# Kernel optimization log

Hardware: AMD Instinct MI355X
Metric: run time of the kernel (lower is better)

## Reference

```python
import jax, jax.numpy as jnp
import numpy as np

B, T, N, H = 256, 64, 128, 128  # batch, seq_len, num_tasks, hidden_dim


def setup_inputs() -> dict:
    key = jax.random.key(0)
    k = jax.random.split(key, 8)
    task_seq = jax.random.randint(k[0], (B, T), 0, N)
    status_seq = jax.random.randint(k[1], (B, T), 0, 3)
    raw = (jax.random.uniform(k[2], (N, N)) < 0.05).astype(jnp.float32)
    adj = raw + jnp.eye(N, dtype=jnp.float32)
    rs = adj.sum(axis=1, keepdims=True)
    adj = adj / jnp.where(rs == 0, 1.0, rs)
    s = np.float32(1.0 / np.sqrt(H))
    emb = jax.random.normal(k[3], (N * 3, H), jnp.float32) * s      # interaction_emb
    W_ih = jax.random.normal(k[4], (3 * H, 2 * H), jnp.float32) * s  # GRUCell weight_ih (r,z,n)
    W_hh = jax.random.normal(k[5], (3 * H, H), jnp.float32) * s      # GRUCell weight_hh
    b_ih = jnp.zeros((3 * H,), jnp.float32)
    b_hh = jnp.zeros((3 * H,), jnp.float32)
    w_pred = jax.random.normal(k[6], (H,), jnp.float32) * s          # predict_layer weight [1,H] -> [H]
    b_pred = jnp.zeros((), jnp.float32)                              # predict_layer bias
    return dict(task_seq=task_seq, status_seq=status_seq, adj=adj, emb=emb,
                W_ih=W_ih, W_hh=W_hh, b_ih=b_ih, b_hh=b_hh,
                w_pred=w_pred, b_pred=b_pred)


def _gru_cell(x, h, W_ih, W_hh, b_ih, b_hh):
    # torch.nn.GRUCell: gates ordered (reset, update, new)
    gi = x @ W_ih.T + b_ih
    gh = h @ W_hh.T + b_hh
    i_r, i_z, i_n = jnp.split(gi, 3, axis=-1)
    h_r, h_z, h_n = jnp.split(gh, 3, axis=-1)
    r = jax.nn.sigmoid(i_r + h_r)
    z = jax.nn.sigmoid(i_z + h_z)
    n = jnp.tanh(i_n + r * h_n)
    return (1.0 - z) * n + z * h


def reference(task_seq, status_seq, adj, emb, W_ih, W_hh, b_ih, b_hh, w_pred, b_pred):
    Bsz, _ = task_seq.shape
    Nt = adj.shape[0]
    Hd = emb.shape[1]
    b_idx = jnp.arange(Bsz)
    h0 = jnp.zeros((Bsz, Nt, Hd), emb.dtype)

    def step(h, ts):
        task, status = ts                                # [B], [B]
        x = emb[task * 3 + status]                       # [B,H] interaction embedding
        # original: full (adj @ h)[b, task]; identical math computing only needed row
        agg = jnp.einsum('bn,bnh->bh', adj[task], h)     # [B,H]
        prev = h[b_idx, task]                            # [B,H]
        new = _gru_cell(jnp.concatenate([x, agg], axis=1), prev, W_ih, W_hh, b_ih, b_hh)
        h = h.at[b_idx, task].set(new)                   # scatter updated target state
        logits = h @ w_pred + b_pred                     # [B,N] predict over all tasks
        return h, logits

    h_final, logits = jax.lax.scan(step, h0, (task_seq.T, status_seq.T))
    return jnp.transpose(logits, (1, 0, 2)), h_final     # ([B,T,N], [B,N,H])
```

## Files before the change

kernel.cpp:

```cpp
#include <hip/hip_runtime.h>

#define B_ 256
#define T_ 64
#define N_ 128
#define H_ 128
#define G3 384
#define K2 256

#define WS_G    0
#define WS_PW   (WS_G + G3*G3)
#define WS_NZC  (WS_PW + K2*G3)
#define WS_NZP  (WS_NZC + 128)

__global__ void __launch_bounds__(384) prep(
        const float* __restrict__ W_ih, const float* __restrict__ W_hh,
        const float* __restrict__ emb,  const float* __restrict__ b_ih,
        const float* __restrict__ adj,  float* __restrict__ ws) {
    const int bid = blockIdx.x;
    if (bid < 384) {
        __shared__ float es[H_];
        const int e = bid, j = threadIdx.x;
        if (j < H_) es[j] = emb[e * H_ + j];
        __syncthreads();
        float acc = b_ih[j];
        const float4* wrow = (const float4*)(W_ih + j * K2);
        #pragma unroll 8
        for (int i = 0; i < 32; ++i) {
            float4 w = wrow[i];
            acc += w.x * es[4*i];
            acc += w.y * es[4*i + 1];
            acc += w.z * es[4*i + 2];
            acc += w.w * es[4*i + 3];
        }
        (ws + WS_G)[e * G3 + j] = acc;
    } else if (bid < 512) {
        __shared__ float row[N_];
        const int r = bid - 384;
        if (threadIdx.x < N_) row[threadIdx.x] = adj[r * N_ + threadIdx.x];
        __syncthreads();
        if (threadIdx.x == 0) {
            int*  nzc = (int*)(ws + WS_NZC);
            int2* nzp = (int2*)(ws + WS_NZP);
            int cnt = 0;
            for (int n = 0; n < N_; ++n) {
                float w = row[n];
                if (w != 0.0f) { nzp[r * N_ + cnt] = make_int2(n, __float_as_int(w)); ++cnt; }
            }
            int cnt4 = (cnt + 3) & ~3;
            for (int i = cnt; i < cnt4; ++i) nzp[r * N_ + i] = make_int2(0, 0);
            nzc[r] = cnt;
        }
    } else {
        const int k = bid - 512, j = threadIdx.x;
        (ws + WS_PW)[k * G3 + j] = (k < H_) ? W_ih[j * K2 + H_ + k]
                                            : W_hh[j * H_ + (k - H_)];
    }
}

__global__ void __launch_bounds__(768, 3) gkt_main(
        const int* __restrict__ task_seq, const int* __restrict__ status_seq,
        const float* __restrict__ b_hh,   const float* __restrict__ w_pred,
        const float* __restrict__ b_pred, const float* __restrict__ ws,
        float* __restrict__ out) {
    __shared__ __align__(16) float h_lds[N_ * H_];
    __shared__ __align__(16) float aggbuf[H_];
    __shared__ float pl[4 * G3];
    __shared__ float red[H_];
    __shared__ float Ll[N_];
    __shared__ int2  nzbuf[N_];
    __shared__ int   nz_cnt;
    __shared__ int   tasks_l[T_], stats_l[T_];

    const int b   = blockIdx.x;
    const int tid = threadIdx.x;
    const int c   = tid / 192;
    const int j2  = tid - c * 192;

    const float* G   = ws + WS_G;
    const float* PW  = ws + WS_PW;
    const int*   nzc = (const int*)(ws + WS_NZC);
    const int2*  nzp = (const int2*)(ws + WS_NZP);

    float wA[64], wB[64];
    {
        const float* baseA = PW + (c * 64) * G3 + j2;
        #pragma unroll
        for (int kk = 0; kk < 64; ++kk) {
            wA[kk] = baseA[kk * G3];
            wB[kk] = baseA[kk * G3 + 192];
        }
    }

    const float bp = b_pred[0];
    const bool gate0 = (tid < 128);
    const bool gate1 = (tid >= 384 && tid < 512);
    const int  tg = gate0 ? tid : (tid - 384);
    float bhr = 0.f, bhz = 0.f, bhn = 0.f, wpt = 0.f;
    if (gate0 || gate1) { bhr = b_hh[tg]; bhz = b_hh[128 + tg]; bhn = b_hh[256 + tg]; }
    if (gate0) wpt = w_pred[tid];

    for (int i = tid; i < N_ * H_; i += 768) h_lds[i] = 0.0f;
    if (tid < T_)          tasks_l[tid]      = task_seq[b * T_ + tid];
    else if (tid < 2*T_)   stats_l[tid - T_] = status_seq[b * T_ + (tid - T_)];
    if (tid >= 128 && tid < 256) { Ll[tid-128] = bp; aggbuf[tid-128] = 0.0f; }
    __syncthreads();

    for (int s = 0; s < T_; ++s) {
        const int task = tasks_l[s];

        float prevreg = 0.f, g0 = 0.f, g1 = 0.f, g2 = 0.f;
        if (gate0 || gate1) {
            prevreg = h_lds[task * H_ + tg];
            const int e = task * 3 + stats_l[s];
            g0 = G[e * G3 + tg];
            g1 = G[e * G3 + 128 + tg];
            g2 = G[e * G3 + 256 + tg];
        }
        {
            const float4* vb = (const float4*)((c < 2) ? (aggbuf + c * 64)
                                                       : (h_lds + task * H_ + (c - 2) * 64));
            float a0 = 0.f, a1 = 0.f, c0 = 0.f, c1 = 0.f;
            #pragma unroll
            for (int i = 0; i < 16; i += 2) {
                const float4 v = vb[i];
                a0 += wA[4*i+0]*v.x; a0 += wA[4*i+1]*v.y; a0 += wA[4*i+2]*v.z; a0 += wA[4*i+3]*v.w;
                c0 += wB[4*i+0]*v.x; c0 += wB[4*i+1]*v.y; c0 += wB[4*i+2]*v.z; c0 += wB[4*i+3]*v.w;
                const float4 u = vb[i+1];
                a1 += wA[4*i+4]*u.x; a1 += wA[4*i+5]*u.y; a1 += wA[4*i+6]*u.z; a1 += wA[4*i+7]*u.w;
                c1 += wB[4*i+4]*u.x; c1 += wB[4*i+5]*u.y; c1 += wB[4*i+6]*u.z; c1 += wB[4*i+7]*u.w;
            }
            pl[c * G3 + j2]       = a0 + a1;
            pl[c * G3 + 192 + j2] = c0 + c1;
        }
        if (tid >= 512 && tid < 640 && s + 1 < T_) {
            const int t = tid - 512, tn = tasks_l[s + 1];
            nzbuf[t] = nzp[tn * N_ + t];
            if (t == 0) nz_cnt = nzc[tn];
        }
        if (tid < 64 && s > 0) {
            float x = red[tid] + red[tid + 64];
            #pragma unroll
            for (int off = 32; off > 0; off >>= 1) x += __shfl_xor(x, off, 64);
            if (tid == 0) Ll[tasks_l[s - 1]] = x + bp;
        }
        __syncthreads();

        if (gate0 || gate1) {
            float sr  = g0 + bhr + pl[tg] + pl[G3 + tg] + pl[2*G3 + tg] + pl[3*G3 + tg];
            float sz  = g1 + bhz + pl[128 + tg] + pl[G3 + 128 + tg]
                                 + pl[2*G3 + 128 + tg] + pl[3*G3 + 128 + tg];
            float in_ = g2 + pl[256 + tg] + pl[G3 + 256 + tg];
            float hn_ = bhn + pl[2*G3 + 256 + tg] + pl[3*G3 + 256 + tg];
            float r = 1.0f / (1.0f + expf(-sr));
            float z = 1.0f / (1.0f + expf(-sz));
            float n = tanhf(in_ + r * hn_);
            float hnew = (1.0f - z) * n + z * prevreg;
            if (gate0) {
                h_lds[task * H_ + tg] = hnew;
                red[tg] = hnew * wpt;
            } else if (s + 1 < T_) {
                float acc = 0.0f;
                const int cnt4 = (nz_cnt + 3) & ~3;
                for (int i = 0; i < cnt4; i += 4) {
                    int2 p0 = nzbuf[i], p1 = nzbuf[i+1], p2 = nzbuf[i+2], p3 = nzbuf[i+3];
                    float h0 = (p0.x == task) ? hnew : h_lds[p0.x * H_ + tg];
                    float h1 = (p1.x == task) ? hnew : h_lds[p1.x * H_ + tg];
                    float h2 = (p2.x == task) ? hnew : h_lds[p2.x * H_ + tg];
                    float h3 = (p3.x == task) ? hnew : h_lds[p3.x * H_ + tg];
                    acc += __int_as_float(p0.y) * h0;
                    acc += __int_as_float(p1.y) * h1;
                    acc += __int_as_float(p2.y) * h2;
                    acc += __int_as_float(p3.y) * h3;
                }
                aggbuf[tg] = acc;
            }
        } else if (tid >= 192 && tid < 320) {
            if (s > 0) out[(size_t)b * T_ * N_ + (size_t)(s - 1) * N_ + (tid - 192)] = Ll[tid - 192];
        }
        __syncthreads();
    }

    if (tid < 64) {
        float x = red[tid] + red[tid + 64];
        #pragma unroll
        for (int off = 32; off > 0; off >>= 1) x += __shfl_xor(x, off, 64);
        if (tid == 0) Ll[tasks_l[T_ - 1]] = x + bp;
    }
    __syncthreads();
    if (tid < N_) out[(size_t)b * T_ * N_ + (size_t)(T_ - 1) * N_ + tid] = Ll[tid];
    {
        float4* dst = (float4*)(out + (size_t)B_ * T_ * N_ + (size_t)b * N_ * H_);
        const float4* src = (const float4*)h_lds;
        for (int i = tid; i < N_ * H_ / 4; i += 768) dst[i] = src[i];
    }
}

extern "C" void kernel_launch(void* const* d_in, const int* in_sizes, int n_in,
                              void* d_out, int out_size, void* d_ws, size_t ws_size,
                              hipStream_t stream) {
    const int*   task = (const int*)d_in[0];
    const int*   stat = (const int*)d_in[1];
    const float* adj  = (const float*)d_in[2];
    const float* emb  = (const float*)d_in[3];
    const float* Wih  = (const float*)d_in[4];
    const float* Whh  = (const float*)d_in[5];
    const float* bih  = (const float*)d_in[6];
    const float* bhh  = (const float*)d_in[7];
    const float* wp   = (const float*)d_in[8];
    const float* bp   = (const float*)d_in[9];
    float* out = (float*)d_out;
    float* ws  = (float*)d_ws;

    prep    <<<768, 384, 0, stream>>>(Wih, Whh, emb, bih, adj, ws);
    gkt_main<<<256, 768, 0, stream>>>(task, stat, bhh, wp, bp, ws, out);
}
```

Before: 216.0 us.

## Repartition GRU matvec across 512 threads with 16-way K split and register weights

Shrinks the block from 768 to 512 threads. Each thread now keeps 192 weights in registers: a 16-row K chunk across 12 output columns. The K reduction moves to 16 partial buffers in LDS, followed by an added reduction phase and an extra barrier per step; the output store and the nz prefetch move into that phase's idle threads. The aim is to cut the number of LDS float4 reads of the input vector and to put the whole K range on fewer waves. In exchange it raises LDS footprint and register pressure, and adds one barrier per timestep.

```diff
diff --git a/kernel.cpp b/kernel.cpp
--- a/kernel.cpp
+++ b/kernel.cpp
@@ -57,14 +57,15 @@
     }
 }
 
-__global__ void __launch_bounds__(768, 3) gkt_main(
+__global__ void __launch_bounds__(512, 2) gkt_main(
         const int* __restrict__ task_seq, const int* __restrict__ status_seq,
         const float* __restrict__ b_hh,   const float* __restrict__ w_pred,
         const float* __restrict__ b_pred, const float* __restrict__ ws,
         float* __restrict__ out) {
     __shared__ __align__(16) float h_lds[N_ * H_];
     __shared__ __align__(16) float aggbuf[H_];
-    __shared__ float pl[4 * G3];
+    __shared__ float pl[16 * G3];
+    __shared__ float gsA[G3], gsB[G3];
     __shared__ float red[H_];
     __shared__ float Ll[N_];
     __shared__ int2  nzbuf[N_];
@@ -73,43 +74,42 @@
 
     const int b   = blockIdx.x;
     const int tid = threadIdx.x;
-    const int c   = tid / 192;
-    const int j2  = tid - c * 192;
+    const int kc  = tid >> 5;
+    const int g   = tid & 31;
 
     const float* G   = ws + WS_G;
     const float* PW  = ws + WS_PW;
     const int*   nzc = (const int*)(ws + WS_NZC);
     const int2*  nzp = (const int2*)(ws + WS_NZP);
 
-    float wA[64], wB[64];
-    {
-        const float* baseA = PW + (c * 64) * G3 + j2;
+    float w[192];
+    #pragma unroll
+    for (int r = 0; r < 12; ++r) {
         #pragma unroll
-        for (int kk = 0; kk < 64; ++kk) {
-            wA[kk] = baseA[kk * G3];
-            wB[kk] = baseA[kk * G3 + 192];
-        }
-    }
+        for (int kk = 0; kk < 16; ++kk)
+            w[r * 16 + kk] = PW[(kc * 16 + kk) * G3 + (g + r * 32)];
+    }
+    #pragma unroll
+    for (int i = 0; i < 192; ++i) asm volatile("" : "+v"(w[i]));
 
     const float bp = b_pred[0];
-    const bool gate0 = (tid < 128);
-    const bool gate1 = (tid >= 384 && tid < 512);
-    const int  tg = gate0 ? tid : (tid - 384);
+    const int tg = tid & 127;
     float bhr = 0.f, bhz = 0.f, bhn = 0.f, wpt = 0.f;
-    if (gate0 || gate1) { bhr = b_hh[tg]; bhz = b_hh[128 + tg]; bhn = b_hh[256 + tg]; }
-    if (gate0) wpt = w_pred[tid];
-
-    for (int i = tid; i < N_ * H_; i += 768) h_lds[i] = 0.0f;
+    if (tid < 256) { bhr = b_hh[tg]; bhz = b_hh[128 + tg]; bhn = b_hh[256 + tg]; }
+    if (tid < 128) wpt = w_pred[tg];
+
+    for (int i = tid; i < N_ * H_; i += 512) h_lds[i] = 0.0f;
     if (tid < T_)          tasks_l[tid]      = task_seq[b * T_ + tid];
     else if (tid < 2*T_)   stats_l[tid - T_] = status_seq[b * T_ + (tid - T_)];
     if (tid >= 128 && tid < 256) { Ll[tid-128] = bp; aggbuf[tid-128] = 0.0f; }
     __syncthreads();
 
+    #pragma unroll 1
     for (int s = 0; s < T_; ++s) {
         const int task = tasks_l[s];
 
         float prevreg = 0.f, g0 = 0.f, g1 = 0.f, g2 = 0.f;
-        if (gate0 || gate1) {
+        if (tid < 256) {
             prevreg = h_lds[task * H_ + tg];
             const int e = task * 3 + stats_l[s];
             g0 = G[e * G3 + tg];
@@ -117,25 +117,19 @@
             g2 = G[e * G3 + 256 + tg];
         }
         {
-            const float4* vb = (const float4*)((c < 2) ? (aggbuf + c * 64)
-                                                       : (h_lds + task * H_ + (c - 2) * 64));
-            float a0 = 0.f, a1 = 0.f, c0 = 0.f, c1 = 0.f;
-            #pragma unroll
-            for (int i = 0; i < 16; i += 2) {
-                const float4 v = vb[i];
-                a0 += wA[4*i+0]*v.x; a0 += wA[4*i+1]*v.y; a0 += wA[4*i+2]*v.z; a0 += wA[4*i+3]*v.w;
-                c0 += wB[4*i+0]*v.x; c0 += wB[4*i+1]*v.y; c0 += wB[4*i+2]*v.z; c0 += wB[4*i+3]*v.w;
-                const float4 u = vb[i+1];
-                a1 += wA[4*i+4]*u.x; a1 += wA[4*i+5]*u.y; a1 += wA[4*i+6]*u.z; a1 += wA[4*i+7]*u.w;
-                c1 += wB[4*i+4]*u.x; c1 += wB[4*i+5]*u.y; c1 += wB[4*i+6]*u.z; c1 += wB[4*i+7]*u.w;
-            }
-            pl[c * G3 + j2]       = a0 + a1;
-            pl[c * G3 + 192 + j2] = c0 + c1;
-        }
-        if (tid >= 512 && tid < 640 && s + 1 < T_) {
-            const int t = tid - 512, tn = tasks_l[s + 1];
-            nzbuf[t] = nzp[tn * N_ + t];
-            if (t == 0) nz_cnt = nzc[tn];
+            const float* vbase = (kc < 8) ? (aggbuf + kc * 16)
+                                          : (h_lds + task * H_ + (kc - 8) * 16);
+            const float4* vb4 = (const float4*)vbase;
+            const float4 v0 = vb4[0], v1 = vb4[1], v2 = vb4[2], v3 = vb4[3];
+            const float vv[16] = {v0.x, v0.y, v0.z, v0.w, v1.x, v1.y, v1.z, v1.w,
+                                  v2.x, v2.y, v2.z, v2.w, v3.x, v3.y, v3.z, v3.w};
+            #pragma unroll
+            for (int r = 0; r < 12; ++r) {
+                float acc = 0.f;
+                #pragma unroll
+                for (int kk = 0; kk < 16; ++kk) acc += w[r * 16 + kk] * vv[kk];
+                pl[kc * G3 + g + r * 32] = acc;
+            }
         }
         if (tid < 64 && s > 0) {
             float x = red[tid] + red[tid + 64];
@@ -145,17 +139,36 @@
         }
         __syncthreads();
 
-        if (gate0 || gate1) {
-            float sr  = g0 + bhr + pl[tg] + pl[G3 + tg] + pl[2*G3 + tg] + pl[3*G3 + tg];
-            float sz  = g1 + bhz + pl[128 + tg] + pl[G3 + 128 + tg]
-                                 + pl[2*G3 + 128 + tg] + pl[3*G3 + 128 + tg];
-            float in_ = g2 + pl[256 + tg] + pl[G3 + 256 + tg];
-            float hn_ = bhn + pl[2*G3 + 256 + tg] + pl[3*G3 + 256 + tg];
+        if (tid < G3) {
+            float sA = pl[tid];
+            #pragma unroll
+            for (int k2 = 1; k2 < 8; ++k2)  sA += pl[k2 * G3 + tid];
+            float sB = pl[8 * G3 + tid];
+            #pragma unroll
+            for (int k2 = 9; k2 < 16; ++k2) sB += pl[k2 * G3 + tid];
+            gsA[tid] = sA;
+            gsB[tid] = sB;
+        } else {
+            const int t = tid - G3;
+            if (s > 0) out[(size_t)b * T_ * N_ + (size_t)(s - 1) * N_ + t] = Ll[t];
+            if (s + 1 < T_) {
+                const int tn = tasks_l[s + 1];
+                nzbuf[t] = nzp[tn * N_ + t];
+                if (t == 0) nz_cnt = nzc[tn];
+            }
+        }
+        __syncthreads();
+
+        if (tid < 256) {
+            float sr  = g0 + bhr + gsA[tg] + gsB[tg];
+            float sz  = g1 + bhz + gsA[128 + tg] + gsB[128 + tg];
+            float in_ = g2 + gsA[256 + tg];
+            float hn_ = bhn + gsB[256 + tg];
             float r = 1.0f / (1.0f + expf(-sr));
             float z = 1.0f / (1.0f + expf(-sz));
             float n = tanhf(in_ + r * hn_);
             float hnew = (1.0f - z) * n + z * prevreg;
-            if (gate0) {
+            if (tid < 128) {
                 h_lds[task * H_ + tg] = hnew;
                 red[tg] = hnew * wpt;
             } else if (s + 1 < T_) {
@@ -174,8 +187,6 @@
                 }
                 aggbuf[tg] = acc;
             }
-        } else if (tid >= 192 && tid < 320) {
-            if (s > 0) out[(size_t)b * T_ * N_ + (size_t)(s - 1) * N_ + (tid - 192)] = Ll[tid - 192];
         }
         __syncthreads();
     }
@@ -191,7 +202,7 @@
     {
         float4* dst = (float4*)(out + (size_t)B_ * T_ * N_ + (size_t)b * N_ * H_);
         const float4* src = (const float4*)h_lds;
-        for (int i = tid; i < N_ * H_ / 4; i += 768) dst[i] = src[i];
+        for (int i = tid; i < N_ * H_ / 4; i += 512) dst[i] = src[i];
     }
 }
 
@@ -212,5 +223,5 @@
     float* ws  = (float*)d_ws;
 
     prep    <<<768, 384, 0, stream>>>(Wih, Whh, emb, bih, adj, ws);
-    gkt_main<<<256, 768, 0, stream>>>(task, stat, bhh, wp, bp, ws, out);
+    gkt_main<<<256, 512, 0, stream>>>(task, stat, bhh, wp, bp, ws, out);
 }
```

New measurement: 218.8 us. Within noise of the previous version (+1.3%).

## Process two batch rows per block and stream GRU weights from global memory

Applied to the files above, without the earlier changes.

Each block now handles two batch elements, with double-sized LDS state, so each weight load feeds two matvecs. The per-thread register-resident weight arrays are removed; weights are instead loaded from global memory (L2/L1) on every step. The grid halves to 128 blocks, which cuts parallelism across CUs, and LDS use doubles to about 140KB per block. The risk is reloading weights every step with fewer blocks in flight, in exchange for lower register pressure and weight reuse across the two sequences.

```diff
diff --git a/kernel.cpp b/kernel.cpp
--- a/kernel.cpp
+++ b/kernel.cpp
@@ -62,136 +62,156 @@
         const float* __restrict__ b_hh,   const float* __restrict__ w_pred,
         const float* __restrict__ b_pred, const float* __restrict__ ws,
         float* __restrict__ out) {
-    __shared__ __align__(16) float h_lds[N_ * H_];
-    __shared__ __align__(16) float aggbuf[H_];
-    __shared__ float pl[4 * G3];
-    __shared__ float red[H_];
-    __shared__ float Ll[N_];
-    __shared__ int2  nzbuf[N_];
-    __shared__ int   nz_cnt;
-    __shared__ int   tasks_l[T_], stats_l[T_];
-
-    const int b   = blockIdx.x;
+    __shared__ __align__(16) float h_lds[2][N_ * H_];
+    __shared__ __align__(16) float aggbuf[2][H_];
+    __shared__ float pl[2][4][G3];
+    __shared__ float red[2][H_];
+    __shared__ float Ll[2][N_];
+    __shared__ int2  nzbuf[2][N_];
+    __shared__ int   nz_cnt[2];
+    __shared__ int   tasks_l[2][T_], stats_l[2][T_];
+
+    const int b0  = blockIdx.x * 2;
     const int tid = threadIdx.x;
-    const int c   = tid / 192;
-    const int j2  = tid - c * 192;
+    const int kc  = tid / 192;
+    const int j2  = tid - kc * 192;
+    const int bt  = (tid >> 7) & 1;
+    const int tg  = tid & 127;
 
     const float* G   = ws + WS_G;
     const float* PW  = ws + WS_PW;
     const int*   nzc = (const int*)(ws + WS_NZC);
     const int2*  nzp = (const int2*)(ws + WS_NZP);
 
-    float wA[64], wB[64];
-    {
-        const float* baseA = PW + (c * 64) * G3 + j2;
-        #pragma unroll
-        for (int kk = 0; kk < 64; ++kk) {
-            wA[kk] = baseA[kk * G3];
-            wB[kk] = baseA[kk * G3 + 192];
-        }
-    }
-
     const float bp = b_pred[0];
-    const bool gate0 = (tid < 128);
-    const bool gate1 = (tid >= 384 && tid < 512);
-    const int  tg = gate0 ? tid : (tid - 384);
     float bhr = 0.f, bhz = 0.f, bhn = 0.f, wpt = 0.f;
-    if (gate0 || gate1) { bhr = b_hh[tg]; bhz = b_hh[128 + tg]; bhn = b_hh[256 + tg]; }
-    if (gate0) wpt = w_pred[tid];
-
-    for (int i = tid; i < N_ * H_; i += 768) h_lds[i] = 0.0f;
-    if (tid < T_)          tasks_l[tid]      = task_seq[b * T_ + tid];
-    else if (tid < 2*T_)   stats_l[tid - T_] = status_seq[b * T_ + (tid - T_)];
-    if (tid >= 128 && tid < 256) { Ll[tid-128] = bp; aggbuf[tid-128] = 0.0f; }
+    if (tid < 512) { bhr = b_hh[tg]; bhz = b_hh[128 + tg]; bhn = b_hh[256 + tg]; }
+    if (tid < 256) wpt = w_pred[tg];
+
+    for (int i = tid; i < 2 * N_ * H_; i += 768) ((float*)h_lds)[i] = 0.0f;
+    if (tid < 64)        tasks_l[0][tid]       = task_seq[(size_t)b0 * T_ + tid];
+    else if (tid < 128)  tasks_l[1][tid - 64]  = task_seq[(size_t)(b0 + 1) * T_ + (tid - 64)];
+    else if (tid < 192)  stats_l[0][tid - 128] = status_seq[(size_t)b0 * T_ + (tid - 128)];
+    else if (tid < 256)  stats_l[1][tid - 192] = status_seq[(size_t)(b0 + 1) * T_ + (tid - 192)];
+    if (tid >= 256 && tid < 512) {
+        const int bb = (tid >> 7) & 1, t = tid & 127;
+        Ll[bb][t] = bp;
+        aggbuf[bb][t] = 0.0f;
+    }
     __syncthreads();
 
+    #pragma unroll 1
     for (int s = 0; s < T_; ++s) {
-        const int task = tasks_l[s];
+        const int task0 = tasks_l[0][s], task1 = tasks_l[1][s];
+        const int taskb = bt ? task1 : task0;
 
         float prevreg = 0.f, g0 = 0.f, g1 = 0.f, g2 = 0.f;
-        if (gate0 || gate1) {
-            prevreg = h_lds[task * H_ + tg];
-            const int e = task * 3 + stats_l[s];
+        if (tid < 512) {
+            prevreg = h_lds[bt][taskb * H_ + tg];
+            const int e = taskb * 3 + stats_l[bt][s];
             g0 = G[e * G3 + tg];
             g1 = G[e * G3 + 128 + tg];
             g2 = G[e * G3 + 256 + tg];
         }
         {
-            const float4* vb = (const float4*)((c < 2) ? (aggbuf + c * 64)
-                                                       : (h_lds + task * H_ + (c - 2) * 64));
-            float a0 = 0.f, a1 = 0.f, c0 = 0.f, c1 = 0.f;
+            const float* wb  = PW + (kc * 64) * G3 + j2;
+            const float* vs0 = (kc < 2) ? (&aggbuf[0][kc * 64])
+                                        : (&h_lds[0][task0 * H_ + (kc - 2) * 64]);
+            const float* vs1 = (kc < 2) ? (&aggbuf[1][kc * 64])
+                                        : (&h_lds[1][task1 * H_ + (kc - 2) * 64]);
+            float aA0 = 0.f, aB0 = 0.f, aA1 = 0.f, aB1 = 0.f;
             #pragma unroll
-            for (int i = 0; i < 16; i += 2) {
-                const float4 v = vb[i];
-                a0 += wA[4*i+0]*v.x; a0 += wA[4*i+1]*v.y; a0 += wA[4*i+2]*v.z; a0 += wA[4*i+3]*v.w;
-                c0 += wB[4*i+0]*v.x; c0 += wB[4*i+1]*v.y; c0 += wB[4*i+2]*v.z; c0 += wB[4*i+3]*v.w;
-                const float4 u = vb[i+1];
-                a1 += wA[4*i+4]*u.x; a1 += wA[4*i+5]*u.y; a1 += wA[4*i+6]*u.z; a1 += wA[4*i+7]*u.w;
-                c1 += wB[4*i+4]*u.x; c1 += wB[4*i+5]*u.y; c1 += wB[4*i+6]*u.z; c1 += wB[4*i+7]*u.w;
-            }
-            pl[c * G3 + j2]       = a0 + a1;
-            pl[c * G3 + 192 + j2] = c0 + c1;
-        }
-        if (tid >= 512 && tid < 640 && s + 1 < T_) {
-            const int t = tid - 512, tn = tasks_l[s + 1];
-            nzbuf[t] = nzp[tn * N_ + t];
-            if (t == 0) nz_cnt = nzc[tn];
-        }
-        if (tid < 64 && s > 0) {
-            float x = red[tid] + red[tid + 64];
+            for (int i = 0; i < 16; ++i) {
+                const float4 u0 = *(const float4*)(vs0 + 4 * i);
+                const float4 u1 = *(const float4*)(vs1 + 4 * i);
+                const float wa0 = wb[(4*i+0)*G3],       wa1 = wb[(4*i+1)*G3];
+                const float wa2 = wb[(4*i+2)*G3],       wa3 = wb[(4*i+3)*G3];
+                const float wc0 = wb[(4*i+0)*G3 + 192], wc1 = wb[(4*i+1)*G3 + 192];
+                const float wc2 = wb[(4*i+2)*G3 + 192], wc3 = wb[(4*i+3)*G3 + 192];
+                aA0 += wa0*u0.x; aA0 += wa1*u0.y; aA0 += wa2*u0.z; aA0 += wa3*u0.w;
+                aB0 += wc0*u0.x; aB0 += wc1*u0.y; aB0 += wc2*u0.z; aB0 += wc3*u0.w;
+                aA1 += wa0*u1.x; aA1 += wa1*u1.y; aA1 += wa2*u1.z; aA1 += wa3*u1.w;
+                aB1 += wc0*u1.x; aB1 += wc1*u1.y; aB1 += wc2*u1.z; aB1 += wc3*u1.w;
+            }
+            pl[0][kc][j2]       = aA0;
+            pl[0][kc][j2 + 192] = aB0;
+            pl[1][kc][j2]       = aA1;
+            pl[1][kc][j2 + 192] = aB1;
+        }
+        if (tid >= 512 && s + 1 < T_) {
+            const int bb = (tid >> 7) & 1, t = tid & 127;
+            const int tn = tasks_l[bb][s + 1];
+            nzbuf[bb][t] = nzp[tn * N_ + t];
+            if (t == 0) nz_cnt[bb] = nzc[tn];
+        }
+        if (tid < 128 && s > 0) {
+            const int bb = tid >> 6, lane = tid & 63;
+            float x = red[bb][lane] + red[bb][lane + 64];
             #pragma unroll
             for (int off = 32; off > 0; off >>= 1) x += __shfl_xor(x, off, 64);
-            if (tid == 0) Ll[tasks_l[s - 1]] = x + bp;
-        }
-        __syncthreads();
-
-        if (gate0 || gate1) {
-            float sr  = g0 + bhr + pl[tg] + pl[G3 + tg] + pl[2*G3 + tg] + pl[3*G3 + tg];
-            float sz  = g1 + bhz + pl[128 + tg] + pl[G3 + 128 + tg]
-                                 + pl[2*G3 + 128 + tg] + pl[3*G3 + 128 + tg];
-            float in_ = g2 + pl[256 + tg] + pl[G3 + 256 + tg];
-            float hn_ = bhn + pl[2*G3 + 256 + tg] + pl[3*G3 + 256 + tg];
+            if (lane == 0) Ll[bb][tasks_l[bb][s - 1]] = x + bp;
+        }
+        __syncthreads();
+
+        if (tid < 512) {
+            float sr  = g0 + bhr + (pl[bt][0][tg] + pl[bt][1][tg])
+                                 + (pl[bt][2][tg] + pl[bt][3][tg]);
+            float sz  = g1 + bhz + (pl[bt][0][128+tg] + pl[bt][1][128+tg])
+                                 + (pl[bt][2][128+tg] + pl[bt][3][128+tg]);
+            float in_ = g2 + (pl[bt][0][256+tg] + pl[bt][1][256+tg]);
+            float hn_ = bhn + (pl[bt][2][256+tg] + pl[bt][3][256+tg]);
             float r = 1.0f / (1.0f + expf(-sr));
             float z = 1.0f / (1.0f + expf(-sz));
             float n = tanhf(in_ + r * hn_);
             float hnew = (1.0f - z) * n + z * prevreg;
-            if (gate0) {
-                h_lds[task * H_ + tg] = hnew;
-                red[tg] = hnew * wpt;
+            if (tid < 256) {
+                h_lds[bt][taskb * H_ + tg] = hnew;
+                red[bt][tg] = hnew * wpt;
             } else if (s + 1 < T_) {
                 float acc = 0.0f;
-                const int cnt4 = (nz_cnt + 3) & ~3;
+                const int cnt4 = (nz_cnt[bt] + 3) & ~3;
                 for (int i = 0; i < cnt4; i += 4) {
-                    int2 p0 = nzbuf[i], p1 = nzbuf[i+1], p2 = nzbuf[i+2], p3 = nzbuf[i+3];
-                    float h0 = (p0.x == task) ? hnew : h_lds[p0.x * H_ + tg];
-                    float h1 = (p1.x == task) ? hnew : h_lds[p1.x * H_ + tg];
-                    float h2 = (p2.x == task) ? hnew : h_lds[p2.x * H_ + tg];
-                    float h3 = (p3.x == task) ? hnew : h_lds[p3.x * H_ + tg];
+                    int2 p0 = nzbuf[bt][i],   p1 = nzbuf[bt][i+1];
+                    int2 p2 = nzbuf[bt][i+2], p3 = nzbuf[bt][i+3];
+                    float h0 = (p0.x == taskb) ? hnew : h_lds[bt][p0.x * H_ + tg];
+                    float h1 = (p1.x == taskb) ? hnew : h_lds[bt][p1.x * H_ + tg];
+                    float h2 = (p2.x == taskb) ? hnew : h_lds[bt][p2.x * H_ + tg];
+                    float h3 = (p3.x == taskb) ? hnew : h_lds[bt][p3.x * H_ + tg];
                     acc += __int_as_float(p0.y) * h0;
                     acc += __int_as_float(p1.y) * h1;
                     acc += __int_as_float(p2.y) * h2;
                     acc += __int_as_float(p3.y) * h3;
                 }
-                aggbuf[tg] = acc;
-            }
-        } else if (tid >= 192 && tid < 320) {
-            if (s > 0) out[(size_t)b * T_ * N_ + (size_t)(s - 1) * N_ + (tid - 192)] = Ll[tid - 192];
-        }
-        __syncthreads();
-    }
-
-    if (tid < 64) {
-        float x = red[tid] + red[tid + 64];
+                aggbuf[bt][tg] = acc;
+            }
+        } else {
+            if (s > 0) {
+                const int bb = (tid >> 7) & 1, t = tid & 127;
+                out[(size_t)(b0 + bb) * T_ * N_ + (size_t)(s - 1) * N_ + t] = Ll[bb][t];
+            }
+        }
+        __syncthreads();
+    }
+
+    if (tid < 128) {
+        const int bb = tid >> 6, lane = tid & 63;
+        float x = red[bb][lane] + red[bb][lane + 64];
         #pragma unroll
         for (int off = 32; off > 0; off >>= 1) x += __shfl_xor(x, off, 64);
-        if (tid == 0) Ll[tasks_l[T_ - 1]] = x + bp;
+        if (lane == 0) Ll[bb][tasks_l[bb][T_ - 1]] = x + bp;
     }
     __syncthreads();
-    if (tid < N_) out[(size_t)b * T_ * N_ + (size_t)(T_ - 1) * N_ + tid] = Ll[tid];
+    if (tid < 256) {
+        out[(size_t)(b0 + bt) * T_ * N_ + (size_t)(T_ - 1) * N_ + tg] = Ll[bt][tg];
+    }
     {
-        float4* dst = (float4*)(out + (size_t)B_ * T_ * N_ + (size_t)b * N_ * H_);
-        const float4* src = (const float4*)h_lds;
-        for (int i = tid; i < N_ * H_ / 4; i += 768) dst[i] = src[i];
+        const size_t hbase = (size_t)B_ * T_ * N_;
+        const int qb = N_ * H_ / 4;
+        for (int i = tid; i < 2 * qb; i += 768) {
+            const int bb = i / qb, r = i - bb * qb;
+            ((float4*)(out + hbase + (size_t)(b0 + bb) * N_ * H_))[r] =
+                ((const float4*)h_lds[bb])[r];
+        }
     }
 }
 
@@ -212,5 +232,5 @@
     float* ws  = (float*)d_ws;
 
     prep    <<<768, 384, 0, stream>>>(Wih, Whh, emb, bih, adj, ws);
-    gkt_main<<<256, 768, 0, stream>>>(task, stat, bhh, wp, bp, ws, out);
+    gkt_main<<<128, 768, 0, stream>>>(task, stat, bhh, wp, bp, ws, out);
 }
```

Result: slower. 273.0 us (+26.4%).
